# Optimization experiments

Hardware: AMD Instinct MI355X
Metric: run time of the kernel (lower is better)

The kernel has to match this reference:

```python
import jax, jax.numpy as jnp
import numpy as np
import math

N = 2048          # rows (forced: input_dim_B // 2)
DB = 4096         # input_dim_B
DA = 5120         # input_dim_A
DX2 = DA - DB     # 1024, X2 feature dim
M1, M2 = 8, 4
DK, DV1, DV2 = 64, 64, 64
M = 512           # d_model of trailing encoder layers (nhead=1 inside)
LN_EPS = 1e-5


def setup_inputs() -> dict:
    key = jax.random.key(0)
    ks = jax.random.split(key, 24)
    s = 0.02
    f32 = jnp.float32
    inp = {
        "X1": jax.random.normal(ks[0], (N, DB), f32),
        "X2": jax.random.normal(ks[1], (N, DX2), f32),
        "X3": jax.random.normal(ks[2], (N, DB), f32),
        # Type-A heads (stacked over m1)
        "WQ": jax.random.normal(ks[3], (M1, DA, DK), f32) * s,
        "WK": jax.random.normal(ks[4], (M1, DA, DK), f32) * s,
        "WV": jax.random.normal(ks[5], (M1, DA, DV1), f32) * s,
        # Type-B heads (stacked over m2)
        "WVB": jax.random.normal(ks[6], (M2, DX2, DV2), f32) * s,
        "W_ali": jax.random.normal(ks[7], (DB, DB // 2), f32) * s,
        "W_O": jax.random.normal(ks[8], (M1 * DV1 + M2 * DV2, M), f32) * s,
        # two TransformerEncoderLayers (post-LN, nhead=1, relu FFN), stacked over layer dim
        "enc_Wq": jax.random.normal(ks[9], (2, M, M), f32) * s,
        "enc_Wk": jax.random.normal(ks[10], (2, M, M), f32) * s,
        "enc_Wv": jax.random.normal(ks[11], (2, M, M), f32) * s,
        "enc_bq": jnp.zeros((2, M), f32),
        "enc_bk": jnp.zeros((2, M), f32),
        "enc_bv": jnp.zeros((2, M), f32),
        "enc_Wo": jax.random.normal(ks[12], (2, M, M), f32) * s,
        "enc_bo": jnp.zeros((2, M), f32),
        "enc_ln1_g": jnp.ones((2, M), f32),
        "enc_ln1_b": jnp.zeros((2, M), f32),
        "enc_W1": jax.random.normal(ks[13], (2, M, DV1), f32) * s,
        "enc_b1": jnp.zeros((2, DV1), f32),
        "enc_W2": jax.random.normal(ks[14], (2, DV1, M), f32) * s,
        "enc_b2": jnp.zeros((2, M), f32),
        "enc_ln2_g": jnp.ones((2, M), f32),
        "enc_ln2_b": jnp.zeros((2, M), f32),
    }
    return inp


def _layer_norm(x, g, b):
    mu = jnp.mean(x, axis=-1, keepdims=True)
    var = jnp.mean(jnp.square(x - mu), axis=-1, keepdims=True)
    return (x - mu) * jax.lax.rsqrt(var + LN_EPS) * g + b


def _encoder_layer(x, Wq, bq, Wk, bk, Wv, bv, Wo, bo, g1, b1, W1, bW1, W2, bW2, g2, b2):
    # post-norm TransformerEncoderLayer, nhead=1, dropout in eval mode (off)
    q = x @ Wq + bq
    k = x @ Wk + bk
    v = x @ Wv + bv
    att = jax.nn.softmax((q @ k.T) / math.sqrt(M), axis=-1) @ v
    x = _layer_norm(x + (att @ Wo + bo), g1, b1)
    f = jax.nn.relu(x @ W1 + bW1) @ W2 + bW2
    return _layer_norm(x + f, g2, b2)


def reference(X1, X2, X3, WQ, WK, WV, WVB, W_ali, W_O,
              enc_Wq, enc_bq, enc_Wk, enc_bk, enc_Wv, enc_bv, enc_Wo, enc_bo,
              enc_ln1_g, enc_ln1_b, enc_W1, enc_b1, enc_W2, enc_b2, enc_ln2_g, enc_ln2_b):
    XA = jnp.concatenate([X1, X2], axis=1)  # [N, DA]
    # Type-A heads, batched over m1
    Q = jnp.einsum('nd,hdk->hnk', XA, WQ)
    K = jnp.einsum('nd,hdk->hnk', XA, WK)
    V = jnp.einsum('nd,hdv->hnv', XA, WV)
    scores = jnp.einsum('hnk,hmk->hnm', Q, K) / math.sqrt(DK)
    S = jax.nn.softmax(scores, axis=1)  # torch softmax(dim=0): over query/row axis
    ZA = jnp.einsum('hnm,hmv->hnv', S, V)             # [m1, N, dv1]
    ZA = jnp.transpose(ZA, (1, 0, 2)).reshape(N, M1 * DV1)
    # Type-B heads
    ali = jax.nn.sigmoid(X3) @ W_ali                  # [N, N] (DB//2 == N)
    zb = jnp.einsum('nd,hdv->hnv', X2, WVB)           # [m2, N, dv2]
    ZB = jnp.einsum('nm,hmv->hnv', ali, zb)
    ZB = jnp.transpose(ZB, (1, 0, 2)).reshape(N, M2 * DV2)
    Z = jnp.concatenate([ZA, ZB], axis=1) @ W_O       # [N, M]
    for l in range(2):
        Z = _encoder_layer(Z, enc_Wq[l], enc_bq[l], enc_Wk[l], enc_bk[l],
                           enc_Wv[l], enc_bv[l], enc_Wo[l], enc_bo[l],
                           enc_ln1_g[l], enc_ln1_b[l], enc_W1[l], enc_b1[l],
                           enc_W2[l], enc_b2[l], enc_ln2_g[l], enc_ln2_b[l])
    return Z
```

## Files before the change

kernel.cpp:

```cpp
#include <hip/hip_runtime.h>

#define DEV __device__ __forceinline__

typedef __attribute__((ext_vector_type(4))) float f32x4;
typedef __attribute__((ext_vector_type(8))) short s16x8;

DEV ushort f2b(float f) {
  union { float f; unsigned u; } x; x.f = f;
  unsigned r = (x.u + 0x7FFFu + ((x.u >> 16) & 1u)) >> 16;
  return (ushort)r;
}
DEV float b2f(ushort u) {
  union { unsigned u; float f; } x; x.u = ((unsigned)u) << 16;
  return x.f;
}

DEV void gload16(const ushort* g, ushort* l) {
  __builtin_amdgcn_global_load_lds(
      (const __attribute__((address_space(1))) unsigned int*)g,
      (__attribute__((address_space(3))) unsigned int*)l, 16, 0, 0);
}

struct PtrList { const float* p[4]; };

template<int BM, int BN, int BIAS, int ACT, bool OF, bool OB, int SKX,
         bool CSTAT, bool RSTAT, int NBUF>
__global__ __launch_bounds__(256) void gemm(
    const ushort* __restrict__ A, int lda, long long sA,
    const ushort* __restrict__ B, int ldb, long long sB,
    float* __restrict__ Cf, ushort* __restrict__ Cb, int ldc, long long sC,
    const float* __restrict__ bias, const float* __restrict__ bias2,
    float* __restrict__ pmo, float* __restrict__ pso,
    float scale0, float scale1, int K)
{
  constexpr int WM = BM / 2, WN = BN / 2, FM = WM / 16, FN = WN / 16;
  __shared__ __align__(16) ushort As[NBUF][BM * 64];
  __shared__ __align__(16) ushort Bs[NBUF][BN * 64];
  const int tid = threadIdx.x, l = tid & 63, w = tid >> 6;
  const int wr = w >> 1, wc = w & 1;
  const int gx = gridDim.x, gy = gridDim.y;
  const int nwg = gx * gy;
  const int orig = blockIdx.y * gx + blockIdx.x;
  const int xcd = orig & 7, rest = orig >> 3;
  const int q8 = nwg >> 3, r8 = nwg & 7;
  const int f = (xcd < r8 ? xcd * (q8 + 1) : r8 * (q8 + 1) + (xcd - r8) * q8) + rest;
  int bxr = f / gy;
  const int byy = f - bxr * gy;
  int ks = 0;
  if constexpr (SKX > 1) {
    const int nbx = gx / SKX;
    ks = bxr / nbx; bxr -= ks * nbx;
  }
  const int brow = byy * BM, bcol = bxr * BN;
  const long long z = blockIdx.z;
  A += z * sA + (size_t)ks * K;
  B += z * sB + (size_t)ks * K;
  const int lr = l & 15;
  const int sw = lr & 7, kh = l >> 4;
  f32x4 acc[FM][FN] = {};
  const int nk = K >> 6;

  auto stage = [&](int kt, int buf) {
    const int kof = kt << 6;
#pragma unroll
    for (int i = 0; i < BM / 32; ++i) {
      const int c = i * 256 + tid;
      const int r = c >> 3, k8 = c & 7;
      gload16(A + (size_t)(brow + r) * lda + kof + ((k8 ^ (r & 7)) << 3),
              &As[buf][i * 2048 + w * 512]);
    }
#pragma unroll
    for (int i = 0; i < BN / 32; ++i) {
      const int c = i * 256 + tid;
      const int r = c >> 3, k8 = c & 7;
      gload16(B + (size_t)(bcol + r) * ldb + kof + ((k8 ^ (r & 7)) << 3),
              &Bs[buf][i * 2048 + w * 512]);
    }
  };

  auto compute = [&](int kt, int buf) {
#pragma unroll
    for (int kk = 0; kk < 2; ++kk) {
      const int koff = ((kk * 4 + kh) ^ sw) << 3;
      s16x8 af[FM], bf[FN];
#pragma unroll
      for (int m = 0; m < FM; ++m)
        af[m] = *(const s16x8*)&As[buf][(wr * WM + m * 16 + lr) * 64 + koff];
#pragma unroll
      for (int n = 0; n < FN; ++n)
        bf[n] = *(const s16x8*)&Bs[buf][(wc * WN + n * 16 + lr) * 64 + koff];
#pragma unroll
      for (int m = 0; m < FM; ++m)
#pragma unroll
        for (int n = 0; n < FN; ++n)
          acc[m][n] = __builtin_amdgcn_mfma_f32_16x16x32_bf16(af[m], bf[n], acc[m][n], 0, 0, 0);
    }
  };

  if constexpr (NBUF == 2) {
    stage(0, 0);
    __syncthreads();
    for (int kt = 0; kt < nk - 1; ++kt) {
      stage(kt + 1, (kt + 1) & 1);
      compute(kt, kt & 1);
      __syncthreads();
    }
    compute(nk - 1, (nk - 1) & 1);
  } else {
    for (int kt = 0; kt < nk; ++kt) {
      stage(kt, 0);
      __syncthreads();
      compute(kt, 0);
      __syncthreads();
    }
  }

  if constexpr (OF || OB) {
    const float sc = (z == 0) ? scale0 : scale1;
    const float* bp = (z == 0) ? bias : bias2;
    const int cr = (l >> 4) * 4, cc = l & 15;
#pragma unroll
    for (int m = 0; m < FM; ++m) {
      const int r0 = brow + wr * WM + m * 16 + cr;
#pragma unroll
      for (int n = 0; n < FN; ++n) {
        const int gc = bcol + wc * WN + n * 16 + cc;
        float bc = 0.f;
        if constexpr (BIAS == 1) bc = bp[gc];
#pragma unroll
        for (int j = 0; j < 4; ++j) {
          float v = acc[m][n][j];
          if constexpr (BIAS == 1) v += bc;
          if constexpr (BIAS == 2) v += bp[r0 + j];
          v *= sc;
          if constexpr (ACT == 1) v = fmaxf(v, 0.f);
          const size_t off = (size_t)(r0 + j) * ldc + gc + (size_t)((z * SKX + ks) * sC);
          if constexpr (OF) Cf[off] = v;
          if constexpr (OB) Cb[off] = f2b(v);
        }
      }
    }
  }

  if constexpr (CSTAT) {
    __shared__ float sM[2][2][FN][16], sS[2][2][FN][16];
    float mx[FN], se[FN];
#pragma unroll
    for (int n = 0; n < FN; ++n) {
      float m0 = -3e38f;
#pragma unroll
      for (int m = 0; m < FM; ++m)
#pragma unroll
        for (int j = 0; j < 4; ++j) m0 = fmaxf(m0, acc[m][n][j]);
      float s0 = 0.f;
#pragma unroll
      for (int m = 0; m < FM; ++m)
#pragma unroll
        for (int j = 0; j < 4; ++j) s0 += __expf(acc[m][n][j] - m0);
      mx[n] = m0; se[n] = s0;
    }
#pragma unroll
    for (int o = 16; o <= 32; o <<= 1) {
#pragma unroll
      for (int n = 0; n < FN; ++n) {
        float m2 = __shfl_xor(mx[n], o), s2 = __shfl_xor(se[n], o);
        float M = fmaxf(mx[n], m2);
        se[n] = se[n] * __expf(mx[n] - M) + s2 * __expf(m2 - M);
        mx[n] = M;
      }
    }
    __syncthreads();
    if (l < 16) {
#pragma unroll
      for (int n = 0; n < FN; ++n) { sM[wr][wc][n][l] = mx[n]; sS[wr][wc][n][l] = se[n]; }
    }
    __syncthreads();
    if (wr == 0 && l < 16) {
#pragma unroll
      for (int n = 0; n < FN; ++n) {
        float m1 = sM[0][wc][n][l], m2 = sM[1][wc][n][l];
        float s1 = sS[0][wc][n][l], s2 = sS[1][wc][n][l];
        float M = fmaxf(m1, m2);
        float S = s1 * __expf(m1 - M) + s2 * __expf(m2 - M);
        const int gc = bcol + wc * 32 + n * 16 + l;
        const size_t o = ((size_t)(z * gy + byy)) * 2048 + gc;
        pmo[o] = M; pso[o] = S;
      }
    }
  }

  if constexpr (RSTAT) {
    __shared__ float sRM[2][2][WM], sRS[2][2][WM];
#pragma unroll
    for (int m = 0; m < FM; ++m) {
#pragma unroll
      for (int j = 0; j < 4; ++j) {
        float m0 = -3e38f;
#pragma unroll
        for (int n = 0; n < FN; ++n) m0 = fmaxf(m0, acc[m][n][j]);
        float s0 = 0.f;
#pragma unroll
        for (int n = 0; n < FN; ++n) s0 += __expf(acc[m][n][j] - m0);
#pragma unroll
        for (int o = 1; o <= 8; o <<= 1) {
          float m2 = __shfl_xor(m0, o), s2 = __shfl_xor(s0, o);
          float M = fmaxf(m0, m2);
          s0 = s0 * __expf(m0 - M) + s2 * __expf(m2 - M);
          m0 = M;
        }
        if ((l & 15) == 0) {
          sRM[wr][wc][m * 16 + (l >> 4) * 4 + j] = m0;
          sRS[wr][wc][m * 16 + (l >> 4) * 4 + j] = s0;
        }
      }
    }
    __syncthreads();
    if (wc == 0) {
      float m1 = sRM[wr][0][l], m2 = sRM[wr][1][l];
      float s1 = sRS[wr][0][l], s2 = sRS[wr][1][l];
      float M = fmaxf(m1, m2);
      float S = s1 * __expf(m1 - M) + s2 * __expf(m2 - M);
      const size_t o = (size_t)bxr * 2048 + brow + wr * WM + l;
      pmo[o] = M; pso[o] = S;
    }
  }
}

__global__ __launch_bounds__(256) void ffn_fused(
    const ushort* __restrict__ X, const ushort* __restrict__ W1,
    const float* __restrict__ b1, const ushort* __restrict__ W2T,
    const float* __restrict__ b2, float* __restrict__ Y)
{
  __shared__ __align__(16) ushort As[64 * 64];
  __shared__ __align__(16) ushort Bs[64 * 64];
  __shared__ __align__(16) ushort Hs[64 * 64];
  const int tid = threadIdx.x, l = tid & 63, w = tid >> 6;
  const int wr = w >> 1, wc = w & 1;
  const int bx = blockIdx.x, brow = blockIdx.y * 64;
  const int lr = l & 15, g = l >> 4, sw = lr & 7;
  f32x4 acc[2][2] = {};
  for (int kt = 0; kt < 8; ++kt) {
    const int kof = kt << 6;
#pragma unroll
    for (int i = 0; i < 2; ++i) {
      const int c = i * 256 + tid, r = c >> 3, k8 = c & 7;
      gload16(X + (size_t)(brow + r) * 512 + kof + ((k8 ^ (r & 7)) << 3),
              &As[i * 2048 + w * 512]);
    }
#pragma unroll
    for (int i = 0; i < 2; ++i) {
      const int c = i * 256 + tid, r = c >> 3, k8 = c & 7;
      gload16(W1 + (size_t)r * 512 + kof + ((k8 ^ (r & 7)) << 3),
              &Bs[i * 2048 + w * 512]);
    }
    __syncthreads();
#pragma unroll
    for (int kk = 0; kk < 2; ++kk) {
      const int koff = ((kk * 4 + g) ^ sw) << 3;
      s16x8 af[2], bf[2];
#pragma unroll
      for (int m = 0; m < 2; ++m) af[m] = *(const s16x8*)&As[(wr * 32 + m * 16 + lr) * 64 + koff];
#pragma unroll
      for (int n = 0; n < 2; ++n) bf[n] = *(const s16x8*)&Bs[(wc * 32 + n * 16 + lr) * 64 + koff];
#pragma unroll
      for (int m = 0; m < 2; ++m)
#pragma unroll
        for (int n = 0; n < 2; ++n)
          acc[m][n] = __builtin_amdgcn_mfma_f32_16x16x32_bf16(af[m], bf[n], acc[m][n], 0, 0, 0);
    }
    __syncthreads();
  }
#pragma unroll
  for (int m = 0; m < 2; ++m)
#pragma unroll
    for (int n = 0; n < 2; ++n) {
      const int col = wc * 32 + n * 16 + lr;
      const float bb = b1[col];
#pragma unroll
      for (int j = 0; j < 4; ++j) {
        const int row = wr * 32 + m * 16 + g * 4 + j;
        Hs[row * 64 + (((col >> 3) ^ (row & 7)) << 3) + (col & 7)] =
            f2b(fmaxf(acc[m][n][j] + bb, 0.f));
      }
    }
#pragma unroll
  for (int i = 0; i < 2; ++i) {
    const int c = i * 256 + tid, r = c >> 3, k8 = c & 7;
    gload16(W2T + (size_t)(bx * 64 + r) * 64 + ((k8 ^ (r & 7)) << 3),
            &Bs[i * 2048 + w * 512]);
  }
  __syncthreads();
  f32x4 acc2[2][2] = {};
#pragma unroll
  for (int kk = 0; kk < 2; ++kk) {
    const int koff = ((kk * 4 + g) ^ sw) << 3;
    s16x8 af[2], bf[2];
#pragma unroll
    for (int m = 0; m < 2; ++m) af[m] = *(const s16x8*)&Hs[(wr * 32 + m * 16 + lr) * 64 + koff];
#pragma unroll
    for (int n = 0; n < 2; ++n) bf[n] = *(const s16x8*)&Bs[(wc * 32 + n * 16 + lr) * 64 + koff];
#pragma unroll
    for (int m = 0; m < 2; ++m)
#pragma unroll
      for (int n = 0; n < 2; ++n)
        acc2[m][n] = __builtin_amdgcn_mfma_f32_16x16x32_bf16(af[m], bf[n], acc2[m][n], 0, 0, 0);
  }
#pragma unroll
  for (int m = 0; m < 2; ++m)
#pragma unroll
    for (int n = 0; n < 2; ++n) {
      const int gc = bx * 64 + wc * 32 + n * 16 + lr;
      const float bb = b2[gc];
#pragma unroll
      for (int j = 0; j < 4; ++j) {
        const int row = brow + wr * 32 + m * 16 + g * 4 + j;
        Y[(size_t)row * 512 + gc] = acc2[m][n][j] + bb;
      }
    }
}

__global__ __launch_bounds__(256) void pv_fused(
    const ushort* __restrict__ Q, const ushort* __restrict__ K,
    const ushort* __restrict__ Vt, const float* __restrict__ lse,
    ushort* __restrict__ ZAP)
{
  __shared__ __align__(16) ushort Qs[64 * 64];
  __shared__ __align__(16) ushort Ks[2][64 * 64];
  __shared__ __align__(16) ushort Vs[2][64 * 64];
  __shared__ __align__(16) ushort Ps[64 * 64];
  __shared__ float Ls[512];
  const int tid = threadIdx.x, l = tid & 63, w = tid >> 6;
  const int wr = w >> 1, wc = w & 1;
  const int h = blockIdx.z, brow = blockIdx.x * 64, ms = blockIdx.y;
  const int lr = l & 15, g = l >> 4, sw = lr & 7;

  auto stageKV = [&](int mc, int buf) {
#pragma unroll
    for (int i = 0; i < 2; ++i) {
      const int c = i * 256 + tid, r = c >> 3, k8 = c & 7;
      gload16(K + (size_t)(mc * 64 + r) * 512 + h * 64 + ((k8 ^ (r & 7)) << 3),
              &Ks[buf][i * 2048 + w * 512]);
    }
#pragma unroll
    for (int i = 0; i < 2; ++i) {
      const int c = i * 256 + tid, r = c >> 3, k8 = c & 7;
      gload16(Vt + (size_t)(h * 64 + r) * 2048 + mc * 64 + ((k8 ^ (r & 7)) << 3),
              &Vs[buf][i * 2048 + w * 512]);
    }
  };

#pragma unroll
  for (int i = 0; i < 2; ++i) {
    const int c = i * 256 + tid, r = c >> 3, k8 = c & 7;
    gload16(Q + (size_t)(brow + r) * 512 + h * 64 + ((k8 ^ (r & 7)) << 3),
            &Qs[i * 2048 + w * 512]);
  }
  stageKV(ms * 8, 0);
  for (int i = tid; i < 512; i += 256) Ls[i] = lse[h * 2048 + ms * 512 + i];
  __syncthreads();

  s16x8 aq[2][2];
#pragma unroll
  for (int nf = 0; nf < 2; ++nf)
#pragma unroll
    for (int kk = 0; kk < 2; ++kk)
      aq[nf][kk] = *(const s16x8*)&Qs[(wr * 32 + nf * 16 + lr) * 64 + (((kk * 4 + g) ^ sw) << 3)];

  f32x4 zacc[2][2] = {};
  for (int mi = 0; mi < 8; ++mi) {
    const int mc = ms * 8 + mi;
    const int buf = mi & 1;
    if (mi < 7) stageKV(mc + 1, buf ^ 1);
    f32x4 sacc[2][2] = {};
#pragma unroll
    for (int kk = 0; kk < 2; ++kk) {
      const int koff = ((kk * 4 + g) ^ sw) << 3;
      s16x8 bk[2];
#pragma unroll
      for (int mf = 0; mf < 2; ++mf)
        bk[mf] = *(const s16x8*)&Ks[buf][(wc * 32 + mf * 16 + lr) * 64 + koff];
#pragma unroll
      for (int nf = 0; nf < 2; ++nf)
#pragma unroll
        for (int mf = 0; mf < 2; ++mf)
          sacc[nf][mf] = __builtin_amdgcn_mfma_f32_16x16x32_bf16(aq[nf][kk], bk[mf], sacc[nf][mf], 0, 0, 0);
    }
#pragma unroll
    for (int nf = 0; nf < 2; ++nf)
#pragma unroll
      for (int mf = 0; mf < 2; ++mf) {
        const int m_loc = wc * 32 + mf * 16 + lr;
        const float lv = Ls[mi * 64 + m_loc];
#pragma unroll
        for (int j = 0; j < 4; ++j) {
          const int n_loc = wr * 32 + nf * 16 + g * 4 + j;
          Ps[n_loc * 64 + (((m_loc >> 3) ^ (n_loc & 7)) << 3) + (m_loc & 7)] =
              f2b(__expf(sacc[nf][mf][j] - lv));
        }
      }
    __syncthreads();
#pragma unroll
    for (int kk = 0; kk < 2; ++kk) {
      const int koff = ((kk * 4 + g) ^ sw) << 3;
      s16x8 pa[2], bv[2];
#pragma unroll
      for (int nf = 0; nf < 2; ++nf)
        pa[nf] = *(const s16x8*)&Ps[(wr * 32 + nf * 16 + lr) * 64 + koff];
#pragma unroll
      for (int vf = 0; vf < 2; ++vf)
        bv[vf] = *(const s16x8*)&Vs[buf][(wc * 32 + vf * 16 + lr) * 64 + koff];
#pragma unroll
      for (int nf = 0; nf < 2; ++nf)
#pragma unroll
        for (int vf = 0; vf < 2; ++vf)
          zacc[nf][vf] = __builtin_amdgcn_mfma_f32_16x16x32_bf16(pa[nf], bv[vf], zacc[nf][vf], 0, 0, 0);
    }
    __syncthreads();
  }
  ushort* out = ZAP + (size_t)ms * 2048 * 512;
#pragma unroll
  for (int nf = 0; nf < 2; ++nf)
#pragma unroll
    for (int vf = 0; vf < 2; ++vf)
#pragma unroll
      for (int j = 0; j < 4; ++j) {
        const int n = brow + wr * 32 + nf * 16 + g * 4 + j;
        const int col = h * 64 + wc * 32 + vf * 16 + lr;
        out[(size_t)n * 512 + col] = f2b(zacc[nf][vf][j]);
      }
}

template<int NS, int ACT>
__global__ __launch_bounds__(256) void reduceN(const ushort* __restrict__ P, long long sC,
    ushort* __restrict__ out, int cols, int ldout, long long zPoff, long long zOoff,
    int cshift, long long bstride, float scale, int scThresh, int rows,
    const float* __restrict__ bias)
{
  P += blockIdx.z * zPoff; out += blockIdx.z * zOoff;
  const int c4n = cols >> 2;
  const size_t total = (size_t)rows * c4n;
  for (size_t i = (size_t)blockIdx.x * 256 + threadIdx.x; i < total; i += (size_t)gridDim.x * 256) {
    const size_t r = i / c4n;
    const int c4 = (int)(i - r * c4n) << 2;
    float4 s = make_float4(0.f, 0.f, 0.f, 0.f);
#pragma unroll
    for (int k = 0; k < NS; ++k) {
      ushort4 t = *(const ushort4*)(P + (size_t)k * sC + r * cols + c4);
      s.x += b2f(t.x); s.y += b2f(t.y); s.z += b2f(t.z); s.w += b2f(t.w);
    }
    if constexpr (ACT == 1) {
      float4 bb = *(const float4*)(bias + c4);
      s.x = fmaxf(s.x + bb.x, 0.f); s.y = fmaxf(s.y + bb.y, 0.f);
      s.z = fmaxf(s.z + bb.z, 0.f); s.w = fmaxf(s.w + bb.w, 0.f);
    }
    const float sc = (c4 < scThresh) ? scale : 1.f;
    ushort4 o;
    o.x = f2b(s.x * sc); o.y = f2b(s.y * sc); o.z = f2b(s.z * sc); o.w = f2b(s.w * sc);
    const size_t oo = r * ldout + (size_t)(c4 >> cshift) * bstride + (c4 & ((1 << cshift) - 1));
    *(ushort4*)(out + oo) = o;
  }
}

__global__ __launch_bounds__(256) void prep_xab(const float* __restrict__ X1,
    const float* __restrict__ X2, ushort* __restrict__ XAb) {
  const size_t total = (size_t)2048 * 1280;
  for (size_t i = (size_t)blockIdx.x * 256 + threadIdx.x; i < total; i += (size_t)gridDim.x * 256) {
    const size_t r = i / 1280;
    const int c = (int)(i - r * 1280) << 2;
    float4 v = (c < 4096) ? *(const float4*)(X1 + r * 4096 + c)
                          : *(const float4*)(X2 + r * 1024 + (c - 4096));
    ushort4 o; o.x = f2b(v.x); o.y = f2b(v.y); o.z = f2b(v.z); o.w = f2b(v.w);
    *(ushort4*)(XAb + r * 5120 + c) = o;
  }
}

__global__ __launch_bounds__(256) void prep_x3w(const float* __restrict__ X3,
    const float* __restrict__ Wali, ushort* __restrict__ sX3,
    ushort* __restrict__ Walib) {
  const size_t n1 = (size_t)2048 * 1024;
  const size_t n2 = (size_t)4096 * 512;
  const size_t total = n1 + n2;
  for (size_t i = (size_t)blockIdx.x * 256 + threadIdx.x; i < total; i += (size_t)gridDim.x * 256) {
    if (i < n1) {
      const size_t r = i / 1024;
      const int c = (int)(i - r * 1024) << 2;
      float4 v = *(const float4*)(X3 + r * 4096 + c);
      v.x = 1.f / (1.f + __expf(-v.x)); v.y = 1.f / (1.f + __expf(-v.y));
      v.z = 1.f / (1.f + __expf(-v.z)); v.w = 1.f / (1.f + __expf(-v.w));
      ushort4 o; o.x = f2b(v.x); o.y = f2b(v.y); o.z = f2b(v.z); o.w = f2b(v.w);
      *(ushort4*)(sX3 + r * 4096 + c) = o;
    } else {
      const size_t j = i - n1;
      const size_t r = j / 512;
      const int c = (int)(j - r * 512) << 2;
      float4 v = *(const float4*)(Wali + r * 2048 + c);
      ushort4 o; o.x = f2b(v.x); o.y = f2b(v.y); o.z = f2b(v.z); o.w = f2b(v.w);
      *(ushort4*)(Walib + r * 2048 + c) = o;
    }
  }
}

__global__ __launch_bounds__(256) void expconv_row(const float* __restrict__ S,
    const float* __restrict__ pm, const float* __restrict__ ps, ushort* __restrict__ P) {
  const int r = blockIdx.x;
  float m = pm[(size_t)(threadIdx.x & 31) * 2048 + r];
  float s = ps[(size_t)(threadIdx.x & 31) * 2048 + r];
#pragma unroll
  for (int o = 1; o < 32; o <<= 1) {
    float m2 = __shfl_xor(m, o), s2 = __shfl_xor(s, o);
    float M = fmaxf(m, m2);
    s = s * __expf(m - M) + s2 * __expf(m2 - M);
    m = M;
  }
  const float L = m + __logf(s);
  const float* row = S + (size_t)r * 2048;
  ushort* pr = P + (size_t)r * 2048;
  for (int c = threadIdx.x * 4; c < 2048; c += 1024) {
    float4 v = *(const float4*)(row + c);
    ushort4 o4;
    o4.x = f2b(__expf(v.x - L)); o4.y = f2b(__expf(v.y - L));
    o4.z = f2b(__expf(v.z - L)); o4.w = f2b(__expf(v.w - L));
    *(ushort4*)(pr + c) = o4;
  }
}

__global__ __launch_bounds__(256) void colcombine(const float* __restrict__ pm,
    const float* __restrict__ ps, float* __restrict__ lse) {
  const int id = blockIdx.x * 256 + threadIdx.x;
  const int h = id >> 11, c = id & 2047;
  float M = -3e38f;
#pragma unroll
  for (int s = 0; s < 16; ++s) M = fmaxf(M, pm[((size_t)(h * 16 + s)) * 2048 + c]);
  float S = 0.f;
#pragma unroll
  for (int s = 0; s < 16; ++s) {
    size_t o = ((size_t)(h * 16 + s)) * 2048 + c;
    S += ps[o] * __expf(pm[o] - M);
  }
  lse[id] = M + __logf(S);
}

__global__ __launch_bounds__(256) void transpose_conv_multi(PtrList in, int zPerT,
    ushort* __restrict__ out, int R, int C) {
  __shared__ ushort t[32][33];
  const int z = blockIdx.z;
  const float* ip = in.p[z / zPerT] + (size_t)(z % zPerT) * R * C;
  ushort* op = out + (size_t)z * R * C;
  const int r0 = blockIdx.x * 32, c0 = blockIdx.y * 32;
#pragma unroll
  for (int i = 0; i < 4; ++i) {
    int r = r0 + threadIdx.y + i * 8;
    int c = c0 + threadIdx.x;
    float v = (r < R && c < C) ? ip[(size_t)r * C + c] : 0.f;
    t[threadIdx.x][threadIdx.y + i * 8] = f2b(v);
  }
  __syncthreads();
#pragma unroll
  for (int i = 0; i < 4; ++i) {
    int c = c0 + threadIdx.y + i * 8;
    int r = r0 + threadIdx.x;
    if (c < C && r < R) op[(size_t)c * R + r] = t[threadIdx.y + i * 8][threadIdx.x];
  }
}

__global__ __launch_bounds__(256) void transpose_conv_batch(
    const float* __restrict__ WVB, ushort* __restrict__ WVBT,
    const float* __restrict__ W_O, ushort* __restrict__ WOT,
    const float* __restrict__ eW1, ushort* __restrict__ EW1T,
    const float* __restrict__ eW2, ushort* __restrict__ EW2T) {
  __shared__ ushort t[32][33];
  const int b = blockIdx.x;
  const float* ip; ushort* op; int R, C, r0, c0;
  if (b < 256) {
    const int h = b >> 6, loc = b & 63;
    ip = WVB + (size_t)h * 65536; op = WVBT + (size_t)h * 65536;
    R = 1024; C = 64; r0 = (loc & 31) * 32; c0 = (loc >> 5) * 32;
  } else if (b < 640) {
    const int loc = b - 256;
    ip = W_O; op = WOT;
    R = 768; C = 512; r0 = (loc % 24) * 32; c0 = (loc / 24) * 32;
  } else if (b < 704) {
    const int loc = b - 640, lyr = loc >> 5, lo = loc & 31;
    ip = eW1 + (size_t)lyr * 32768; op = EW1T + (size_t)lyr * 32768;
    R = 512; C = 64; r0 = (lo & 15) * 32; c0 = (lo >> 4) * 32;
  } else {
    const int loc = b - 704, lyr = loc >> 5, lo = loc & 31;
    ip = eW2 + (size_t)lyr * 32768; op = EW2T + (size_t)lyr * 32768;
    R = 64; C = 512; r0 = (lo & 1) * 32; c0 = (lo >> 1) * 32;
  }
#pragma unroll
  for (int i = 0; i < 4; ++i) {
    int r = r0 + threadIdx.y + i * 8;
    int c = c0 + threadIdx.x;
    float v = (r < R && c < C) ? ip[(size_t)r * C + c] : 0.f;
    t[threadIdx.x][threadIdx.y + i * 8] = f2b(v);
  }
  __syncthreads();
#pragma unroll
  for (int i = 0; i < 4; ++i) {
    int c = c0 + threadIdx.y + i * 8;
    int r = r0 + threadIdx.x;
    if (c < C && r < R) op[(size_t)c * R + r] = t[threadIdx.y + i * 8][threadIdx.x];
  }
}

__global__ __launch_bounds__(256) void transpose_b16(const ushort* __restrict__ in,
    ushort* __restrict__ out, int R, int C) {
  __shared__ ushort t[32][33];
  const int r0 = blockIdx.x * 32, c0 = blockIdx.y * 32;
#pragma unroll
  for (int i = 0; i < 4; ++i)
    t[threadIdx.x][threadIdx.y + i * 8] = in[(size_t)(r0 + threadIdx.y + i * 8) * C + c0 + threadIdx.x];
  __syncthreads();
#pragma unroll
  for (int i = 0; i < 4; ++i)
    out[(size_t)(c0 + threadIdx.y + i * 8) * R + r0 + threadIdx.x] = t[threadIdx.y + i * 8][threadIdx.x];
}

__global__ __launch_bounds__(256) void ln_add(const float* __restrict__ X,
    const float* __restrict__ Y, const float* __restrict__ g, const float* __restrict__ b,
    float* __restrict__ of, ushort* __restrict__ ob) {
  const int r = blockIdx.x, t = threadIdx.x;
  const size_t base = (size_t)r * 512;
  float v0 = X[base + t] + Y[base + t];
  float v1 = X[base + t + 256] + Y[base + t + 256];
  float s = v0 + v1;
#pragma unroll
  for (int o = 1; o < 64; o <<= 1) s += __shfl_xor(s, o);
  __shared__ float sm[4], sq[4];
  const int l = t & 63, w = t >> 6;
  if (l == 0) sm[w] = s;
  __syncthreads();
  const float mu = (sm[0] + sm[1] + sm[2] + sm[3]) * (1.f / 512.f);
  const float d0 = v0 - mu, d1 = v1 - mu;
  float q = d0 * d0 + d1 * d1;
#pragma unroll
  for (int o = 1; o < 64; o <<= 1) q += __shfl_xor(q, o);
  if (l == 0) sq[w] = q;
  __syncthreads();
  const float var = (sq[0] + sq[1] + sq[2] + sq[3]) * (1.f / 512.f);
  const float rs = rsqrtf(var + 1e-5f);
  const float o0 = d0 * rs * g[t] + b[t];
  const float o1 = d1 * rs * g[t + 256] + b[t + 256];
  if (of) { of[base + t] = o0; of[base + t + 256] = o1; }
  if (ob) { ob[base + t] = f2b(o0); ob[base + t + 256] = f2b(o1); }
}

extern "C" void kernel_launch(void* const* d_in, const int* in_sizes, int n_in,
                              void* d_out, int out_size, void* d_ws, size_t ws_size,
                              hipStream_t stream) {
  (void)in_sizes; (void)n_in; (void)out_size;
  const float* X1   = (const float*)d_in[0];
  const float* X2   = (const float*)d_in[1];
  const float* X3   = (const float*)d_in[2];
  const float* WQ   = (const float*)d_in[3];
  const float* WK   = (const float*)d_in[4];
  const float* WV   = (const float*)d_in[5];
  const float* WVB  = (const float*)d_in[6];
  const float* Wali = (const float*)d_in[7];
  const float* W_O  = (const float*)d_in[8];
  const float* eWq  = (const float*)d_in[9];
  const float* eWk  = (const float*)d_in[10];
  const float* eWv  = (const float*)d_in[11];
  const float* ebq  = (const float*)d_in[12];
  const float* ebk  = (const float*)d_in[13];
  const float* ebv  = (const float*)d_in[14];
  const float* eWo  = (const float*)d_in[15];
  const float* ebo  = (const float*)d_in[16];
  const float* eg1  = (const float*)d_in[17];
  const float* ebl1 = (const float*)d_in[18];
  const float* eW1  = (const float*)d_in[19];
  const float* eB1  = (const float*)d_in[20];
  const float* eW2  = (const float*)d_in[21];
  const float* eB2  = (const float*)d_in[22];
  const float* eg2  = (const float*)d_in[23];
  const float* ebl2 = (const float*)d_in[24];
  float* OUT = (float*)d_out;
  char* ws = (char*)d_ws;

  const size_t oQB   = 0;
  const size_t oKB   = 2097152;
  const size_t oVB   = 4194304;
  const size_t oVTB  = 6291456;
  const size_t oZAB  = 8388608;
  const size_t oWOT  = 11534336;
  const size_t oEWQT = 12320768;
  const size_t oEWVT = 14417920;
  const size_t oEWOT = 15466496;
  const size_t oEW1T = 16515072;
  const size_t oEW2T = 16646144;
  const size_t oWVBT = 16777216;
  const size_t oZBT  = 17301504;
  const size_t oZ    = 18350080;
  const size_t oZB16 = 22544384;
  const size_t oX2F  = 24641536;
  const size_t oX2B  = 28835840;
  const size_t oY    = 30932992;
  const size_t oATT  = 35127296;
  const size_t oPM   = 37486592;
  const size_t oPS   = 38535168;
  const size_t oLSE  = 39583744;
  const size_t oDYN  = 39649280;
  const size_t oWQT  = oDYN;
  const size_t oQKVP = oDYN + 15728640;
  const size_t oZBP  = oDYN;
  const size_t oSX3  = oDYN;
  const size_t oWAB  = oDYN + 16777216;
  const size_t oW2P  = oDYN + 33554432;
  const size_t oW2T  = oDYN + 50331648;
  const size_t oZAP  = oDYN;
  const size_t oSCFe = oDYN;
  const size_t oPbe  = oDYN + 16777216;
  const size_t oATTP = oDYN + 50331648;
  if (ws_size < oDYN + 67108864) return;

  ushort* XAb  = (ushort*)(ws + oZ);
  ushort* WQT  = (ushort*)(ws + oWQT);
  ushort* QKVP = (ushort*)(ws + oQKVP);
  ushort* ZBP  = (ushort*)(ws + oZBP);
  ushort* sX3  = (ushort*)(ws + oSX3);
  ushort* Walib= (ushort*)(ws + oWAB);
  ushort* W2P  = (ushort*)(ws + oW2P);
  ushort* W2Tb = (ushort*)(ws + oW2T);
  ushort* ZBP2 = (ushort*)(ws + oW2P);
  ushort* ZAP  = (ushort*)(ws + oZAP);
  float*  SCFe = (float*)(ws + oSCFe);
  ushort* Pbe  = (ushort*)(ws + oPbe);
  ushort* ATTP = (ushort*)(ws + oATTP);
  ushort* Qb   = (ushort*)(ws + oQB);
  ushort* Kb   = (ushort*)(ws + oKB);
  ushort* Vb   = (ushort*)(ws + oVB);
  ushort* Vtb  = (ushort*)(ws + oVTB);
  ushort* ZABb = (ushort*)(ws + oZAB);
  ushort* WOT  = (ushort*)(ws + oWOT);
  ushort* EWQT = (ushort*)(ws + oEWQT);
  ushort* EWVT = (ushort*)(ws + oEWVT);
  ushort* EWOT = (ushort*)(ws + oEWOT);
  ushort* EW1T = (ushort*)(ws + oEW1T);
  ushort* EW2T = (ushort*)(ws + oEW2T);
  ushort* WVBT = (ushort*)(ws + oWVBT);
  ushort* ZBT  = (ushort*)(ws + oZBT);
  float*  Zf   = (float*)(ws + oZ);
  ushort* Zb16 = (ushort*)(ws + oZB16);
  float*  X2f  = (float*)(ws + oX2F);
  ushort* X2b  = (ushort*)(ws + oX2B);
  float*  Yf   = (float*)(ws + oY);
  ushort* ATTb = (ushort*)(ws + oATT);
  float*  PM   = (float*)(ws + oPM);
  float*  PS   = (float*)(ws + oPS);
  float*  LSE  = (float*)(ws + oLSE);

  const dim3 tb(32, 8);
  const float rs512 = 0.044194173824159216f;

  prep_xab<<<2048, 256, 0, stream>>>(X1, X2, XAb);
  {
    PtrList wqkv; wqkv.p[0] = WQ; wqkv.p[1] = WK; wqkv.p[2] = WV; wqkv.p[3] = nullptr;
    transpose_conv_multi<<<dim3(160, 2, 24), tb, 0, stream>>>(wqkv, 8, WQT, 5120, 64);
    PtrList enc4; enc4.p[0] = eWq; enc4.p[1] = eWk; enc4.p[2] = eWv; enc4.p[3] = eWo;
    transpose_conv_multi<<<dim3(16, 16, 8), tb, 0, stream>>>(enc4, 2, EWQT, 512, 512);
  }
  transpose_conv_batch<<<768, tb, 0, stream>>>(WVB, WVBT, W_O, WOT, eW1, EW1T, eW2, EW2T);

  gemm<128,128,0,0,false,true,4,false,false,1><<<dim3(48,16,1), 256, 0, stream>>>(
      XAb, 5120, 0, WQT, 5120, 0, nullptr, QKVP, 1536, 3145728LL,
      nullptr, nullptr, nullptr, nullptr, 1.f, 1.f, 1280);
  reduceN<4,0><<<1024, 256, 0, stream>>>(QKVP, 3145728LL, Qb, 1536, 512, 0, 0,
      9, 1048576LL, 0.125f, 512, 2048, nullptr);
  transpose_b16<<<dim3(64, 16), tb, 0, stream>>>(Vb, Vtb, 2048, 512);
  gemm<64,64,0,0,false,true,4,false,false,1><<<dim3(128,4,1), 256, 0, stream>>>(
      WVBT, 1024, 0, XAb + 4096, 5120, 0, nullptr, ZBP, 2048, 524288LL,
      nullptr, nullptr, nullptr, nullptr, 1.f, 1.f, 256);
  reduceN<4,0><<<1024, 256, 0, stream>>>(ZBP, 524288LL, ZBT, 2048, 2048, 0, 0,
      30, 0, 1.f, 0, 256, nullptr);

  prep_x3w<<<2048, 256, 0, stream>>>(X3, Wali, sX3, Walib);
  gemm<128,128,0,0,false,true,4,false,false,2><<<dim3(128,2,1), 256, 0, stream>>>(
      ZBT, 2048, 0, Walib, 2048, 0, nullptr, W2P, 4096, 1048576LL,
      nullptr, nullptr, nullptr, nullptr, 1.f, 1.f, 512);
  reduceN<4,0><<<512, 256, 0, stream>>>(W2P, 1048576LL, W2Tb, 4096, 4096, 0, 0,
      30, 0, 1.f, 0, 256, nullptr);
  gemm<128,64,0,0,false,true,8,false,false,1><<<dim3(32,16,1), 256, 0, stream>>>(
      sX3, 4096, 0, W2Tb, 4096, 0, nullptr, ZBP2, 256, 524288LL,
      nullptr, nullptr, nullptr, nullptr, 1.f, 1.f, 512);
  reduceN<8,0><<<512, 256, 0, stream>>>(ZBP2, 524288LL, ZABb + 512, 256, 768, 0, 0,
      30, 0, 1.f, 0, 2048, nullptr);

  gemm<128,64,0,0,false,false,1,true,false,1><<<dim3(32,16,8), 256, 0, stream>>>(
      Qb, 512, 64, Kb, 512, 64, nullptr, nullptr, 2048, 0,
      nullptr, nullptr, PM, PS, 1.f, 1.f, 64);
  colcombine<<<64, 256, 0, stream>>>(PM, PS, LSE);
  pv_fused<<<dim3(32, 4, 8), 256, 0, stream>>>(Qb, Kb, Vtb, LSE, ZAP);
  reduceN<4,0><<<1024, 256, 0, stream>>>(ZAP, 1048576LL, ZABb, 512, 768, 0, 0,
      30, 0, 1.f, 0, 2048, nullptr);

  gemm<64,64,0,0,true,true,1,false,false,2><<<dim3(8,32,1), 256, 0, stream>>>(
      ZABb, 768, 0, WOT, 768, 0, Zf, Zb16, 512, 0,
      nullptr, nullptr, nullptr, nullptr, 1.f, 1.f, 768);

  for (int lyr = 0; lyr < 2; ++lyr) {
    const ushort* wq = EWQT + (size_t)lyr * 262144;
    const ushort* wv = EWVT + (size_t)lyr * 262144;
    const ushort* wo = EWOT + (size_t)lyr * 262144;
    const ushort* w1 = EW1T + (size_t)lyr * 32768;
    const ushort* w2 = EW2T + (size_t)lyr * 32768;
    gemm<128,64,1,0,false,true,1,false,false,2><<<dim3(8,16,2), 256, 0, stream>>>(
        Zb16, 512, 0, wq, 512, 524288LL, nullptr, Qb, 512, 1048576LL,
        ebq + lyr * 512, ebk + lyr * 512, nullptr, nullptr, rs512, 1.f, 512);
    gemm<64,64,2,0,false,true,1,false,false,2><<<dim3(32,8,1), 256, 0, stream>>>(
        wv, 512, 0, Zb16, 512, 0, nullptr, Vtb, 2048, 0,
        ebv + lyr * 512, nullptr, nullptr, nullptr, 1.f, 1.f, 512);
    gemm<128,64,0,0,true,false,1,false,true,1><<<dim3(32,16,1), 256, 0, stream>>>(
        Qb, 512, 0, Kb, 512, 0, SCFe, nullptr, 2048, 0,
        nullptr, nullptr, PM, PS, 1.f, 1.f, 512);
    expconv_row<<<2048, 256, 0, stream>>>(SCFe, PM, PS, Pbe);
    gemm<128,64,0,0,false,true,4,false,false,1><<<dim3(32,16,1), 256, 0, stream>>>(
        Pbe, 2048, 0, Vtb, 2048, 0, nullptr, ATTP, 512, 1048576LL,
        nullptr, nullptr, nullptr, nullptr, 1.f, 1.f, 512);
    reduceN<4,0><<<1024, 256, 0, stream>>>(ATTP, 1048576LL, ATTb, 512, 512, 0, 0,
        30, 0, 1.f, 0, 2048, nullptr);
    gemm<64,64,1,0,true,false,1,false,false,2><<<dim3(8,32,1), 256, 0, stream>>>(
        ATTb, 512, 0, wo, 512, 0, Yf, nullptr, 512, 0,
        ebo + lyr * 512, nullptr, nullptr, nullptr, 1.f, 1.f, 512);
    ln_add<<<2048, 256, 0, stream>>>(Zf, Yf, eg1 + lyr * 512, ebl1 + lyr * 512, X2f, X2b);
    ffn_fused<<<dim3(8, 32), 256, 0, stream>>>(
        X2b, w1, eB1 + lyr * 64, w2, eB2 + lyr * 512, Yf);
    ln_add<<<2048, 256, 0, stream>>>(X2f, Yf, eg2 + lyr * 512, ebl2 + lyr * 512,
                                     (lyr == 0) ? Zf : OUT, (lyr == 0) ? Zb16 : nullptr);
  }
}
```

Before: 356.1 us.

## Add 256x256-tile ping-pong GEMM kernel for QKV projection with split-K five

Introduces a new 512-thread GEMM kernel using 256x256 output tiles, double-buffered LDS via direct global-to-LDS loads, a phased MFMA schedule with barriers and priority hints, and XCD-aware block remapping. It replaces the 128x128 split-K=4 GEMM for the QKV projection with this kernel at split-K=5 (Kc=1024), and the reduction now sums five partials. Larger tiles raise arithmetic intensity and cut global traffic. The cost is fewer workgroups (240) and more partial-sum traffic from the extra split.

```diff
diff --git a/kernel.cpp b/kernel.cpp
--- a/kernel.cpp
+++ b/kernel.cpp
@@ -224,6 +224,152 @@
       pmo[o] = M; pso[o] = S;
     }
   }
+}
+
+struct Frag8 { int dummy; };
+
+template<int MH, int NH, bool RA, bool RB>
+DEV void phase_read(const ushort* __restrict__ Asb, const ushort* __restrict__ Bsb,
+                    int arow, int brw, int kh, int sw,
+                    s16x8 (&af)[2][4], s16x8 (&bfh)[2][2][2]) {
+  if constexpr (RA) {
+#pragma unroll
+    for (int kk = 0; kk < 2; ++kk) {
+      const int koff = ((kk * 4 + kh) ^ sw) << 3;
+#pragma unroll
+      for (int m = 0; m < 4; ++m)
+        af[kk][m] = *(const s16x8*)&Asb[MH * 8192 + (arow + m * 16) * 64 + koff];
+    }
+  }
+  if constexpr (RB) {
+#pragma unroll
+    for (int kk = 0; kk < 2; ++kk) {
+      const int koff = ((kk * 4 + kh) ^ sw) << 3;
+#pragma unroll
+      for (int n = 0; n < 2; ++n)
+        bfh[NH][kk][n] = *(const s16x8*)&Bsb[NH * 8192 + (brw + n * 16) * 64 + koff];
+    }
+  }
+}
+
+template<int MH, int NH>
+DEV void qmfma(const s16x8 (&af)[2][4], const s16x8 (&bfh)[2][2][2],
+               f32x4 (&acc)[8][4]) {
+#pragma unroll
+  for (int kk = 0; kk < 2; ++kk)
+#pragma unroll
+    for (int m = 0; m < 4; ++m)
+#pragma unroll
+      for (int n = 0; n < 2; ++n)
+        acc[MH * 4 + m][NH * 2 + n] = __builtin_amdgcn_mfma_f32_16x16x32_bf16(
+            af[kk][m], bfh[NH][kk][n], acc[MH * 4 + m][NH * 2 + n], 0, 0, 0);
+}
+
+DEV void tailwait(int c) {
+  if (c == 1) { asm volatile("s_waitcnt vmcnt(4)" ::: "memory"); }
+  else if (c == 2) { asm volatile("s_waitcnt vmcnt(0)" ::: "memory"); }
+}
+
+template<int NBX>
+__global__ __launch_bounds__(512, 2) void gemm256(
+    const ushort* __restrict__ A, int lda,
+    const ushort* __restrict__ B, int ldb,
+    ushort* __restrict__ Cb, int ldc, long long sC, int Kc)
+{
+  __shared__ __align__(16) ushort As[2][2][8192];
+  __shared__ __align__(16) ushort Bs[2][2][8192];
+  const int tid = threadIdx.x, l = tid & 63, w = tid >> 6;
+  const int wr = w >> 2, wc = w & 3;
+  const int gx = gridDim.x, gy = gridDim.y;
+  const int nwg = gx * gy;
+  const int orig = blockIdx.y * gx + blockIdx.x;
+  const int xcd = orig & 7, rest = orig >> 3;
+  const int q8 = nwg >> 3, r8 = nwg & 7;
+  const int f = (xcd < r8 ? xcd * (q8 + 1) : r8 * (q8 + 1) + (xcd - r8) * q8) + rest;
+  int bxr = f / gy;
+  const int byy = f - bxr * gy;
+  const int ks = bxr / NBX; bxr -= ks * NBX;
+  const int brow = byy * 256, bcol = bxr * 256;
+  A += (size_t)ks * Kc;
+  B += (size_t)ks * Kc;
+  const int nk = Kc >> 6;
+  const int lr = l & 15, kh = l >> 4, sw = lr & 7;
+  const int arow = wr * 64 + lr, brw = wc * 32 + lr;
+
+  const int r0 = tid >> 3, k80 = tid & 7;
+  const size_t aoff = (size_t)(brow + r0) * lda + ((k80 ^ (r0 & 7)) << 3);
+  const size_t boff = (size_t)(bcol + r0) * ldb + ((k80 ^ (r0 & 7)) << 3);
+
+  f32x4 acc[8][4] = {};
+  s16x8 af[2][4];
+  s16x8 bfh[2][2][2];
+
+  auto stA = [&](int kt, int buf, int half) {
+    if (kt >= nk) return;
+    const ushort* s = A + aoff + (size_t)(half * 128) * lda + (kt << 6);
+    gload16(s, &As[buf][half][w * 512]);
+    gload16(s + (size_t)64 * lda, &As[buf][half][4096 + w * 512]);
+  };
+  auto stB = [&](int kt, int buf, int half) {
+    if (kt >= nk) return;
+    const ushort* s = B + boff + (size_t)(half * 128) * ldb + (kt << 6);
+    gload16(s, &Bs[buf][half][w * 512]);
+    gload16(s + (size_t)64 * ldb, &Bs[buf][half][4096 + w * 512]);
+  };
+
+  stA(0, 0, 0); stB(0, 0, 0); stA(0, 0, 1); stB(0, 0, 1);
+  stA(1, 1, 0); stB(1, 1, 0);
+  asm volatile("s_waitcnt vmcnt(4)" ::: "memory");
+  asm volatile("s_barrier" ::: "memory");
+
+#define PH(BUF, MH, NH, RA, RB, STG, TW) do {                                  \
+    phase_read<MH, NH, RA, RB>(&As[BUF][0][0], &Bs[BUF][0][0],                 \
+                               arow, brw, kh, sw, af, bfh);                    \
+    STG;                                                                       \
+    asm volatile("s_barrier" ::: "memory");                                    \
+    asm volatile("s_waitcnt lgkmcnt(0)" ::: "memory");                         \
+    __builtin_amdgcn_sched_barrier(0);                                         \
+    __builtin_amdgcn_s_setprio(1);                                             \
+    qmfma<MH, NH>(af, bfh, acc);                                               \
+    __builtin_amdgcn_s_setprio(0);                                             \
+    tailwait(TW);                                                              \
+    asm volatile("s_barrier" ::: "memory");                                    \
+  } while (0)
+
+  const int NT2 = nk >> 1;
+#pragma unroll 1
+  for (int j = 0; j < NT2; ++j) {
+    const int t1 = 2 * j + 1, t2 = 2 * j + 2, t3 = 2 * j + 3;
+    const int tw4 = (t2 < nk) ? 1 : 2;
+    const int tw8 = (t2 < nk) ? 1 : 0;
+    PH(0, 0, 0, true,  true,  stA(t1, 1, 1), 0);
+    PH(0, 0, 1, false, true,  stB(t1, 1, 1), 0);
+    PH(0, 1, 0, true,  false, stA(t2, 0, 0), 0);
+    PH(0, 1, 1, false, false, stB(t2, 0, 0), tw4);
+    PH(1, 0, 0, true,  true,  stA(t2, 0, 1), 0);
+    PH(1, 0, 1, false, true,  stB(t2, 0, 1), 0);
+    PH(1, 1, 0, true,  false, stA(t3, 1, 0), 0);
+    PH(1, 1, 1, false, false, stB(t3, 1, 0), tw8);
+  }
+#undef PH
+
+  ushort* out = Cb + (size_t)ks * sC;
+  const int cr = kh * 4, cc = lr;
+#pragma unroll
+  for (int mh = 0; mh < 2; ++mh)
+#pragma unroll
+    for (int m = 0; m < 4; ++m) {
+      const int ro = brow + mh * 128 + wr * 64 + m * 16 + cr;
+#pragma unroll
+      for (int nh = 0; nh < 2; ++nh)
+#pragma unroll
+        for (int n = 0; n < 2; ++n) {
+          const int gc = bcol + nh * 128 + wc * 32 + n * 16 + cc;
+#pragma unroll
+          for (int j2 = 0; j2 < 4; ++j2)
+            out[(size_t)(ro + j2) * ldc + gc] = f2b(acc[mh * 4 + m][nh * 2 + n][j2]);
+        }
+    }
 }
 
 __global__ __launch_bounds__(256) void ffn_fused(
@@ -762,10 +908,9 @@
   }
   transpose_conv_batch<<<768, tb, 0, stream>>>(WVB, WVBT, W_O, WOT, eW1, EW1T, eW2, EW2T);
 
-  gemm<128,128,0,0,false,true,4,false,false,1><<<dim3(48,16,1), 256, 0, stream>>>(
-      XAb, 5120, 0, WQT, 5120, 0, nullptr, QKVP, 1536, 3145728LL,
-      nullptr, nullptr, nullptr, nullptr, 1.f, 1.f, 1280);
-  reduceN<4,0><<<1024, 256, 0, stream>>>(QKVP, 3145728LL, Qb, 1536, 512, 0, 0,
+  gemm256<6><<<dim3(30, 8, 1), 512, 0, stream>>>(
+      XAb, 5120, WQT, 5120, QKVP, 1536, 3145728LL, 1024);
+  reduceN<5,0><<<1024, 256, 0, stream>>>(QKVP, 3145728LL, Qb, 1536, 512, 0, 0,
       9, 1048576LL, 0.125f, 512, 2048, nullptr);
   transpose_b16<<<dim3(64, 16), tb, 0, stream>>>(Vb, Vtb, 2048, 512);
   gemm<64,64,0,0,false,true,4,false,false,1><<<dim3(128,4,1), 256, 0, stream>>>(
```

New measurement: 354.6 us. About the same (-0.4%).
